# Optimization experiments

Hardware: AMD Instinct MI355X
Metric: run time of the kernel (lower is better)

The kernel has to match this reference:

```python
import jax, jax.numpy as jnp
import numpy as np

B = 65536
IN_F = 512
OUT_F = 256
NUM_GROUPS = 8
EPS = 1e-5


def setup_inputs() -> dict:
    key = jax.random.key(0)
    ks = jax.random.split(key, 6)
    return {
        "x": jax.random.normal(ks[0], (B, IN_F), dtype=jnp.float32),
        "weight": jax.random.normal(ks[1], (OUT_F, IN_F), dtype=jnp.float32) * 0.05,
        "bias_linear": jax.random.normal(ks[2], (OUT_F,), dtype=jnp.float32) * 0.05,
        "weight_gn": jax.random.normal(ks[3], (OUT_F,), dtype=jnp.float32),
        "bias_gn": jax.random.normal(ks[4], (OUT_F,), dtype=jnp.float32),
        "bias": jax.random.normal(ks[5], (1, OUT_F, 1, 1), dtype=jnp.float32),
    }


def reference(x, weight, bias_linear, weight_gn, bias_gn, bias):
    # Linear: (B, IN_F) @ (IN_F, OUT_F) + bias -> (B, OUT_F)
    h = jnp.einsum("bi,oi->bo", x, weight) + bias_linear
    # GroupNorm over channel dim (dim=1) with NUM_GROUPS groups
    g = h.reshape(B, NUM_GROUPS, OUT_F // NUM_GROUPS)
    mean = jnp.mean(g, axis=2, keepdims=True)
    var = jnp.mean(jnp.square(g - mean), axis=2, keepdims=True)
    gn = ((g - mean) * jax.lax.rsqrt(var + EPS)).reshape(B, OUT_F)
    gn = gn * weight_gn + bias_gn
    # Min over channels, keepdim -> (B, 1)
    min_vals = jnp.min(gn, axis=1, keepdims=True)
    # torch broadcasting: (B,1) + (1,256,1,1) -> (1,256,B,1)
    result = min_vals + bias
    return result
```

## Files before the change

### kernel.cpp

```cpp
#include <hip/hip_runtime.h>
#include <hip/hip_bf16.h>

#define B_ROWS 65536
#define K_DIM  512
#define N_DIM  256
#define EPS    1e-5f
#define MTILE  32
#define NBLK   512
#define STRIDE 520

using short8  = __attribute__((ext_vector_type(8))) short;
using floatx4 = __attribute__((ext_vector_type(4))) float;

__device__ __forceinline__ unsigned short f2bf(float f) {
    unsigned u = __builtin_bit_cast(unsigned, f);
    u += 0x7FFFu + ((u >> 16) & 1u);
    return (unsigned short)(u >> 16);
}

__global__ __launch_bounds__(64) void pack_w(const float* __restrict__ W,
                                             unsigned short* __restrict__ P) {
    int b    = blockIdx.x;
    int nt   = b >> 4, kk = b & 15;
    int lane = threadIdx.x;
    int l15  = lane & 15, quad = lane >> 4;
    const float* src = W + (size_t)(nt * 16 + l15) * K_DIM + kk * 32 + quad * 8;
    short8 v;
#pragma unroll
    for (int j = 0; j < 8; ++j) v[j] = (short)f2bf(src[j]);
    *(short8*)(P + ((size_t)(nt * 16 + kk) * 64 + lane) * 8) = v;
}

__global__ __launch_bounds__(512, 2) void fused_persistent(
    const float* __restrict__ X, const unsigned short* __restrict__ P,
    const float* __restrict__ bias_lin, const float* __restrict__ wgn,
    const float* __restrict__ bgn, const float* __restrict__ bias,
    float* __restrict__ out)
{
    __shared__ unsigned short Ash[MTILE * STRIDE];
    __shared__ float sm_min[8][MTILE];
    __shared__ float m_sh[MTILE];

    const int tid  = threadIdx.x;
    const int wave = tid >> 6, lane = tid & 63;
    const int l15  = lane & 15, quad = lane >> 4;

    short8 bfr[2][16];
#pragma unroll
    for (int ct = 0; ct < 2; ++ct)
#pragma unroll
        for (int kkg = 0; kkg < 16; ++kkg) {
            int nt = 2 * wave + ct;
            bfr[ct][kkg] = *(const short8*)(P + (((size_t)nt * 16 + kkg) * 64 + lane) * 8);
        }

    float blr[2][4], wgr[2][4], bgr[2][4];
#pragma unroll
    for (int ct = 0; ct < 2; ++ct)
#pragma unroll
        for (int reg = 0; reg < 4; ++reg) {
            int c = wave * 32 + ct * 16 + quad * 4 + reg;
            blr[ct][reg] = bias_lin[c];
            wgr[ct][reg] = wgn[c];
            bgr[ct][reg] = bgn[c];
        }
    float bias_r[4];
#pragma unroll
    for (int pass = 0; pass < 4; ++pass) bias_r[pass] = bias[pass * 64 + (tid >> 3)];

    const int r0 = tid >> 7;
    const int c4 = (tid & 127) * 4;

    const int tiles = B_ROWS / MTILE;
    int t = blockIdx.x;

    float4 xq[8];
#pragma unroll
    for (int p = 0; p < 8; ++p)
        xq[p] = *(const float4*)(X + (size_t)(t * MTILE + r0 + 4 * p) * K_DIM + c4);

    for (; t < tiles; t += NBLK) {
#pragma unroll
        for (int p = 0; p < 8; ++p) {
            ushort4 h;
            h.x = f2bf(xq[p].x); h.y = f2bf(xq[p].y);
            h.z = f2bf(xq[p].z); h.w = f2bf(xq[p].w);
            *(ushort4*)(&Ash[(r0 + 4 * p) * STRIDE + c4]) = h;
        }
        __syncthreads();

        int tn = t + NBLK;
        if (tn < tiles) {
#pragma unroll
            for (int p = 0; p < 8; ++p)
                xq[p] = *(const float4*)(X + (size_t)(tn * MTILE + r0 + 4 * p) * K_DIM + c4);
        }

        floatx4 acc[2][2];
#pragma unroll
        for (int rt = 0; rt < 2; ++rt)
#pragma unroll
            for (int ct = 0; ct < 2; ++ct)
#pragma unroll
                for (int reg = 0; reg < 4; ++reg)
                    acc[rt][ct][reg] = blr[ct][reg];
#pragma unroll
        for (int kk = 0; kk < 16; ++kk) {
            short8 a0 = *(const short8*)&Ash[(l15)      * STRIDE + kk * 32 + quad * 8];
            short8 a1 = *(const short8*)&Ash[(16 + l15) * STRIDE + kk * 32 + quad * 8];
            acc[0][0] = __builtin_amdgcn_mfma_f32_16x16x32_bf16(bfr[0][kk], a0, acc[0][0], 0, 0, 0);
            acc[0][1] = __builtin_amdgcn_mfma_f32_16x16x32_bf16(bfr[1][kk], a0, acc[0][1], 0, 0, 0);
            acc[1][0] = __builtin_amdgcn_mfma_f32_16x16x32_bf16(bfr[0][kk], a1, acc[1][0], 0, 0, 0);
            acc[1][1] = __builtin_amdgcn_mfma_f32_16x16x32_bf16(bfr[1][kk], a1, acc[1][1], 0, 0, 0);
        }

#pragma unroll
        for (int rt = 0; rt < 2; ++rt) {
            float s = 0.f, ss = 0.f;
#pragma unroll
            for (int ct = 0; ct < 2; ++ct)
#pragma unroll
                for (int reg = 0; reg < 4; ++reg) {
                    float v = acc[rt][ct][reg];
                    s += v; ss = fmaf(v, v, ss);
                }
            s  += __shfl_xor(s, 16);  s  += __shfl_xor(s, 32);
            ss += __shfl_xor(ss, 16); ss += __shfl_xor(ss, 32);
            float mean = s * (1.0f / 32.0f);
            float var  = ss * (1.0f / 32.0f) - mean * mean;
            float inv  = rsqrtf(var + EPS);
            float mi   = mean * inv;
            float mn   = 1e30f;
#pragma unroll
            for (int ct = 0; ct < 2; ++ct)
#pragma unroll
                for (int reg = 0; reg < 4; ++reg) {
                    float tnorm = fmaf(acc[rt][ct][reg], inv, -mi);
                    float g = fmaf(tnorm, wgr[ct][reg], bgr[ct][reg]);
                    mn = fminf(mn, g);
                }
            mn = fminf(mn, __shfl_xor(mn, 16));
            mn = fminf(mn, __shfl_xor(mn, 32));
            if (quad == 0) sm_min[wave][rt * 16 + l15] = mn;
        }
        __syncthreads();
        if (tid < MTILE) {
            float m0 = sm_min[0][tid];
#pragma unroll
            for (int w = 1; w < 8; ++w) m0 = fminf(m0, sm_min[w][tid]);
            m_sh[tid] = m0;
        }
        __syncthreads();

        float4 mv = *(const float4*)&m_sh[(tid & 7) * 4];
#pragma unroll
        for (int pass = 0; pass < 4; ++pass) {
            int c = pass * 64 + (tid >> 3);
            float bc = bias_r[pass];
            float4 o;
            o.x = mv.x + bc; o.y = mv.y + bc; o.z = mv.z + bc; o.w = mv.w + bc;
            *(float4*)(out + (size_t)c * B_ROWS + t * MTILE + (tid & 7) * 4) = o;
        }
    }
}

extern "C" void kernel_launch(void* const* d_in, const int* in_sizes, int n_in,
                              void* d_out, int out_size, void* d_ws, size_t ws_size,
                              hipStream_t stream) {
    const float* x    = (const float*)d_in[0];
    const float* w    = (const float*)d_in[1];
    const float* bl   = (const float*)d_in[2];
    const float* wg   = (const float*)d_in[3];
    const float* bg   = (const float*)d_in[4];
    const float* bias = (const float*)d_in[5];

    unsigned short* P = (unsigned short*)d_ws;
    float* out = (float*)d_out;

    hipLaunchKernelGGL(pack_w, dim3(256), dim3(64), 0, stream, w, P);
    hipLaunchKernelGGL(fused_persistent, dim3(NBLK), dim3(512), 0, stream,
                       x, P, bl, wg, bg, bias, out);
}
```

Measured before the change: 232.6 us.

## Use 1024-thread blocks with 16 waves and double-buffered LDS X tiles

The persistent kernel moves to 256 blocks of 1024 threads, so each of the 16 waves owns one 16-column weight tile and holds half as many B-fragment registers. Because each GroupNorm group now spans two waves, partial sums and sums of squares are exchanged through shared memory, which adds a barrier per tile. The bf16 X tile is double-buffered in LDS: the next tile is converted and written while the current one feeds the MFMAs, and the global load runs two tiles ahead. This aims to overlap global loads and conversion with compute and to lower register pressure, at the cost of more LDS use, more barriers and fewer resident blocks.

```diff
diff --git a/kernel.cpp b/kernel.cpp
--- a/kernel.cpp
+++ b/kernel.cpp
@@ -6,7 +6,8 @@
 #define N_DIM  256
 #define EPS    1e-5f
 #define MTILE  32
-#define NBLK   512
+#define NBLK   256
+#define TILES  (B_ROWS / MTILE)
 #define STRIDE 520
 
 using short8  = __attribute__((ext_vector_type(8))) short;
@@ -31,136 +32,144 @@
     *(short8*)(P + ((size_t)(nt * 16 + kk) * 64 + lane) * 8) = v;
 }
 
-__global__ __launch_bounds__(512, 2) void fused_persistent(
+__global__ __launch_bounds__(1024) void fused_persistent(
     const float* __restrict__ X, const unsigned short* __restrict__ P,
     const float* __restrict__ bias_lin, const float* __restrict__ wgn,
     const float* __restrict__ bgn, const float* __restrict__ bias,
     float* __restrict__ out)
 {
-    __shared__ unsigned short Ash[MTILE * STRIDE];
-    __shared__ float sm_min[8][MTILE];
+    __shared__ unsigned short Ash[2][MTILE * STRIDE];
+    __shared__ float smS[16][32];
+    __shared__ float smSS[16][32];
+    __shared__ float smin[16][32];
     __shared__ float m_sh[MTILE];
 
     const int tid  = threadIdx.x;
-    const int wave = tid >> 6, lane = tid & 63;
+    const int wave = tid >> 6;
+    const int lane = tid & 63;
     const int l15  = lane & 15, quad = lane >> 4;
 
-    short8 bfr[2][16];
+    short8 bfr[16];
 #pragma unroll
-    for (int ct = 0; ct < 2; ++ct)
+    for (int kkg = 0; kkg < 16; ++kkg)
+        bfr[kkg] = *(const short8*)(P + (((size_t)wave * 16 + kkg) * 64 + lane) * 8);
+
+    float blr[4], wgr[4], bgr[4];
 #pragma unroll
-        for (int kkg = 0; kkg < 16; ++kkg) {
-            int nt = 2 * wave + ct;
-            bfr[ct][kkg] = *(const short8*)(P + (((size_t)nt * 16 + kkg) * 64 + lane) * 8);
+    for (int r = 0; r < 4; ++r) {
+        int c = wave * 16 + quad * 4 + r;
+        blr[r] = bias_lin[c]; wgr[r] = wgn[c]; bgr[r] = bgn[c];
+    }
+    const float bias_c = bias[tid >> 2];
+
+    const int r0 = (tid >> 7) * 4;
+    const int c4 = (tid & 127) * 4;
+
+    int t = blockIdx.x;
+
+    float4 xq[4];
+#pragma unroll
+    for (int p = 0; p < 4; ++p)
+        xq[p] = *(const float4*)(X + (size_t)(t * MTILE + r0 + p) * K_DIM + c4);
+#pragma unroll
+    for (int p = 0; p < 4; ++p) {
+        ushort4 h;
+        h.x = f2bf(xq[p].x); h.y = f2bf(xq[p].y);
+        h.z = f2bf(xq[p].z); h.w = f2bf(xq[p].w);
+        *(ushort4*)(&Ash[0][(r0 + p) * STRIDE + c4]) = h;
+    }
+    if (t + NBLK < TILES) {
+#pragma unroll
+        for (int p = 0; p < 4; ++p)
+            xq[p] = *(const float4*)(X + (size_t)((t + NBLK) * MTILE + r0 + p) * K_DIM + c4);
+    }
+    __syncthreads();
+
+    int cur = 0;
+    for (; t < TILES; t += NBLK) {
+        if (t + NBLK < TILES) {
+#pragma unroll
+            for (int p = 0; p < 4; ++p) {
+                ushort4 h;
+                h.x = f2bf(xq[p].x); h.y = f2bf(xq[p].y);
+                h.z = f2bf(xq[p].z); h.w = f2bf(xq[p].w);
+                *(ushort4*)(&Ash[cur ^ 1][(r0 + p) * STRIDE + c4]) = h;
+            }
+            if (t + 2 * NBLK < TILES) {
+#pragma unroll
+                for (int p = 0; p < 4; ++p)
+                    xq[p] = *(const float4*)(X + (size_t)((t + 2 * NBLK) * MTILE + r0 + p) * K_DIM + c4);
+            }
         }
 
-    float blr[2][4], wgr[2][4], bgr[2][4];
-#pragma unroll
-    for (int ct = 0; ct < 2; ++ct)
-#pragma unroll
-        for (int reg = 0; reg < 4; ++reg) {
-            int c = wave * 32 + ct * 16 + quad * 4 + reg;
-            blr[ct][reg] = bias_lin[c];
-            wgr[ct][reg] = wgn[c];
-            bgr[ct][reg] = bgn[c];
-        }
-    float bias_r[4];
-#pragma unroll
-    for (int pass = 0; pass < 4; ++pass) bias_r[pass] = bias[pass * 64 + (tid >> 3)];
-
-    const int r0 = tid >> 7;
-    const int c4 = (tid & 127) * 4;
-
-    const int tiles = B_ROWS / MTILE;
-    int t = blockIdx.x;
-
-    float4 xq[8];
-#pragma unroll
-    for (int p = 0; p < 8; ++p)
-        xq[p] = *(const float4*)(X + (size_t)(t * MTILE + r0 + 4 * p) * K_DIM + c4);
-
-    for (; t < tiles; t += NBLK) {
-#pragma unroll
-        for (int p = 0; p < 8; ++p) {
-            ushort4 h;
-            h.x = f2bf(xq[p].x); h.y = f2bf(xq[p].y);
-            h.z = f2bf(xq[p].z); h.w = f2bf(xq[p].w);
-            *(ushort4*)(&Ash[(r0 + 4 * p) * STRIDE + c4]) = h;
-        }
-        __syncthreads();
-
-        int tn = t + NBLK;
-        if (tn < tiles) {
-#pragma unroll
-            for (int p = 0; p < 8; ++p)
-                xq[p] = *(const float4*)(X + (size_t)(tn * MTILE + r0 + 4 * p) * K_DIM + c4);
-        }
-
-        floatx4 acc[2][2];
+        floatx4 acc[2];
 #pragma unroll
         for (int rt = 0; rt < 2; ++rt)
 #pragma unroll
-            for (int ct = 0; ct < 2; ++ct)
-#pragma unroll
-                for (int reg = 0; reg < 4; ++reg)
-                    acc[rt][ct][reg] = blr[ct][reg];
+            for (int r = 0; r < 4; ++r) acc[rt][r] = blr[r];
 #pragma unroll
         for (int kk = 0; kk < 16; ++kk) {
-            short8 a0 = *(const short8*)&Ash[(l15)      * STRIDE + kk * 32 + quad * 8];
-            short8 a1 = *(const short8*)&Ash[(16 + l15) * STRIDE + kk * 32 + quad * 8];
-            acc[0][0] = __builtin_amdgcn_mfma_f32_16x16x32_bf16(bfr[0][kk], a0, acc[0][0], 0, 0, 0);
-            acc[0][1] = __builtin_amdgcn_mfma_f32_16x16x32_bf16(bfr[1][kk], a0, acc[0][1], 0, 0, 0);
-            acc[1][0] = __builtin_amdgcn_mfma_f32_16x16x32_bf16(bfr[0][kk], a1, acc[1][0], 0, 0, 0);
-            acc[1][1] = __builtin_amdgcn_mfma_f32_16x16x32_bf16(bfr[1][kk], a1, acc[1][1], 0, 0, 0);
+            short8 a0 = *(const short8*)&Ash[cur][(l15)      * STRIDE + kk * 32 + quad * 8];
+            short8 a1 = *(const short8*)&Ash[cur][(16 + l15) * STRIDE + kk * 32 + quad * 8];
+            acc[0] = __builtin_amdgcn_mfma_f32_16x16x32_bf16(bfr[kk], a0, acc[0], 0, 0, 0);
+            acc[1] = __builtin_amdgcn_mfma_f32_16x16x32_bf16(bfr[kk], a1, acc[1], 0, 0, 0);
         }
 
+        float sreg[2], ssreg[2];
 #pragma unroll
         for (int rt = 0; rt < 2; ++rt) {
             float s = 0.f, ss = 0.f;
 #pragma unroll
-            for (int ct = 0; ct < 2; ++ct)
-#pragma unroll
-                for (int reg = 0; reg < 4; ++reg) {
-                    float v = acc[rt][ct][reg];
-                    s += v; ss = fmaf(v, v, ss);
-                }
+            for (int r = 0; r < 4; ++r) { float v = acc[rt][r]; s += v; ss = fmaf(v, v, ss); }
             s  += __shfl_xor(s, 16);  s  += __shfl_xor(s, 32);
             ss += __shfl_xor(ss, 16); ss += __shfl_xor(ss, 32);
-            float mean = s * (1.0f / 32.0f);
-            float var  = ss * (1.0f / 32.0f) - mean * mean;
+            sreg[rt] = s; ssreg[rt] = ss;
+            if (quad == 0) { smS[wave][rt * 16 + l15] = s; smSS[wave][rt * 16 + l15] = ss; }
+        }
+        __syncthreads();
+
+#pragma unroll
+        for (int rt = 0; rt < 2; ++rt) {
+            int row = rt * 16 + l15;
+            float st   = sreg[rt]  + smS[wave ^ 1][row];
+            float sst  = ssreg[rt] + smSS[wave ^ 1][row];
+            float mean = st * (1.0f / 32.0f);
+            float var  = sst * (1.0f / 32.0f) - mean * mean;
             float inv  = rsqrtf(var + EPS);
             float mi   = mean * inv;
             float mn   = 1e30f;
 #pragma unroll
-            for (int ct = 0; ct < 2; ++ct)
-#pragma unroll
-                for (int reg = 0; reg < 4; ++reg) {
-                    float tnorm = fmaf(acc[rt][ct][reg], inv, -mi);
-                    float g = fmaf(tnorm, wgr[ct][reg], bgr[ct][reg]);
-                    mn = fminf(mn, g);
-                }
+            for (int r = 0; r < 4; ++r) {
+                float g = fmaf(fmaf(acc[rt][r], inv, -mi), wgr[r], bgr[r]);
+                mn = fminf(mn, g);
+            }
             mn = fminf(mn, __shfl_xor(mn, 16));
             mn = fminf(mn, __shfl_xor(mn, 32));
-            if (quad == 0) sm_min[wave][rt * 16 + l15] = mn;
+            if (quad == 0) smin[wave][row] = mn;
         }
         __syncthreads();
+
         if (tid < MTILE) {
-            float m0 = sm_min[0][tid];
+            float m0 = smin[0][tid];
 #pragma unroll
-            for (int w = 1; w < 8; ++w) m0 = fminf(m0, sm_min[w][tid]);
+            for (int w = 1; w < 16; ++w) m0 = fminf(m0, smin[w][tid]);
             m_sh[tid] = m0;
         }
         __syncthreads();
 
-        float4 mv = *(const float4*)&m_sh[(tid & 7) * 4];
-#pragma unroll
-        for (int pass = 0; pass < 4; ++pass) {
-            int c = pass * 64 + (tid >> 3);
-            float bc = bias_r[pass];
-            float4 o;
-            o.x = mv.x + bc; o.y = mv.y + bc; o.z = mv.z + bc; o.w = mv.w + bc;
-            *(float4*)(out + (size_t)c * B_ROWS + t * MTILE + (tid & 7) * 4) = o;
+        {
+            int c  = tid >> 2;
+            int j0 = (tid & 3) * 8;
+            float4 ma = *(const float4*)&m_sh[j0];
+            float4 mb = *(const float4*)&m_sh[j0 + 4];
+            float4 oa, ob;
+            oa.x = ma.x + bias_c; oa.y = ma.y + bias_c; oa.z = ma.z + bias_c; oa.w = ma.w + bias_c;
+            ob.x = mb.x + bias_c; ob.y = mb.y + bias_c; ob.z = mb.z + bias_c; ob.w = mb.w + bias_c;
+            float* dst = out + (size_t)c * B_ROWS + t * MTILE + j0;
+            *(float4*)dst       = oa;
+            *(float4*)(dst + 4) = ob;
         }
+        cur ^= 1;
     }
 }
 
@@ -178,6 +187,6 @@
     float* out = (float*)d_out;
 
     hipLaunchKernelGGL(pack_w, dim3(256), dim3(64), 0, stream, w, P);
-    hipLaunchKernelGGL(fused_persistent, dim3(NBLK), dim3(512), 0, stream,
+    hipLaunchKernelGGL(fused_persistent, dim3(NBLK), dim3(1024), 0, stream,
                        x, P, bl, wg, bg, bias, out);
 }
```

New measurement: 229.9 us. Within noise of the previous version (-1.1%).
